# Kernel tuning notes

Hardware: AMD Instinct MI355X
Metric: run time of the kernel (lower is better)

The kernel has to match this reference:

```python
import jax, jax.numpy as jnp
import numpy as np
import itertools

KS = 5           # kernel_size per pseudo dim
PDIM = 2         # pseudo-coordinate dim
N_NODES = 50000
N_EDGES = 800000
D_IN = 128
D_OUT = 128
EPS = 1e-12


def l2norm(x):
    n = jnp.linalg.norm(x, axis=-1, keepdims=True)
    return x / jnp.maximum(n, EPS)


def spline_conv(x, src, dst, pseudo, weight, bias):
    """torch_spline_conv with degree=1, open splines, aggr='mean', no root weight."""
    N = x.shape[0]
    out_dim = weight.shape[-1]
    dim = pseudo.shape[1]
    v = pseudo * (KS - 1)                                   # [E, dim] in [0, KS-1)
    i0 = jnp.clip(jnp.floor(v), 0, KS - 2).astype(jnp.int32)
    frac = v - i0.astype(v.dtype)                           # [E, dim]
    # Precompute per-kernel transforms once per node: cheaper than per-edge GEMV
    Xk = jnp.einsum('ni,kio->nko', x, weight)               # [N, K=25, out]
    E = src.shape[0]
    y = jnp.zeros((E, out_dim), x.dtype)
    for bits in itertools.product((0, 1), repeat=dim):      # S = 2**dim = 4 combos
        b = jnp.ones((E,), x.dtype)
        wi = jnp.zeros((E,), jnp.int32)
        stride = 1
        for d, bit in enumerate(bits):
            b = b * (frac[:, d] if bit else 1.0 - frac[:, d])
            wi = wi + (i0[:, d] + bit) * stride
            stride *= KS
        y = y + b[:, None] * Xk[src, wi]                    # gather-weight per edge
    agg = jax.ops.segment_sum(y, dst, num_segments=N)       # scatter-add to targets
    deg = jax.ops.segment_sum(jnp.ones((E,), x.dtype), dst, num_segments=N)
    return agg / jnp.maximum(deg, 1.0)[:, None] + bias      # mean aggregation


def setup_inputs() -> dict:
    key = jax.random.key(0)
    ks = jax.random.split(key, 6)
    K = KS ** PDIM
    x = jax.random.normal(ks[0], (N_NODES, D_IN), jnp.float32)
    edge_index = jax.random.randint(ks[1], (2, N_EDGES), 0, N_NODES, jnp.int32)
    edge_attr = jax.random.uniform(ks[2], (N_EDGES, PDIM), jnp.float32)
    s0 = 1.0 / np.sqrt(K * D_IN)
    s1 = 1.0 / np.sqrt(K * D_OUT)
    w0 = jax.random.normal(ks[3], (K, D_IN, D_OUT), jnp.float32) * s0
    w1 = jax.random.normal(ks[4], (K, D_OUT, D_OUT), jnp.float32) * s1
    b0 = jnp.zeros((D_OUT,), jnp.float32)
    b1 = jnp.zeros((D_OUT,), jnp.float32)
    return {"x": x, "edge_index": edge_index, "edge_attr": edge_attr,
            "w0": w0, "b0": b0, "w1": w1, "b1": b1}


def reference(x, edge_index, edge_attr, w0, b0, w1, b1):
    src, dst = edge_index[0], edge_index[1]
    xs = [l2norm(x)]
    h = x
    for w, b in ((w0, b0), (w1, b1)):
        h = spline_conv(h, src, dst, edge_attr, w, b)
        xs.append(l2norm(h))
        h = jax.nn.relu(h)
    return jnp.concatenate(xs, axis=-1)                     # [N, D_IN + 2*D_OUT]
```

## Files before the change

### kernel.cpp

```cpp
#include <hip/hip_runtime.h>

#define D     128
#define OD    384
#define NK    25
#define KCMAX 13
#define KB0   13

typedef __attribute__((ext_vector_type(8))) short bf16x8;
typedef __attribute__((ext_vector_type(4))) float f32x4;
typedef __attribute__((ext_vector_type(4))) unsigned int u32x4;
typedef const __attribute__((address_space(1))) void gv_t;
typedef __attribute__((address_space(3))) void lv_t;

struct __align__(16) Rec {
  int src;
  unsigned int wi;
  unsigned int b01;
  unsigned int b23;
};

__device__ inline unsigned short f2bf(float f) {
  unsigned int u = __float_as_uint(f);
  u += 0x7fffu + ((u >> 16) & 1u);
  return (unsigned short)(u >> 16);
}
__device__ inline unsigned short f2h(float f) {
  return __builtin_bit_cast(unsigned short, (_Float16)f);
}
__device__ inline float h2f(unsigned int bits16) {
  return (float)__builtin_bit_cast(_Float16, (unsigned short)(bits16 & 0xffffu));
}


__device__ inline int edge_cls(int w00) {
  return (w00 + 6 < KB0) ? 0 : ((w00 >= KB0) ? 2 : 1);
}

__global__ __launch_bounds__(256) void count3_kernel(const int* __restrict__ dstA,
    const float* __restrict__ attr, int E, int* __restrict__ deg,
    int* __restrict__ cnt3) {
  int e = blockIdx.x * 256 + threadIdx.x;
  if (e >= E) return;
  int d = dstA[e];
  atomicAdd(&deg[d], 1);
  float v0 = attr[2 * e] * 4.0f;
  float v1 = attr[2 * e + 1] * 4.0f;
  int i0 = min(3, max(0, (int)v0));
  int i1 = min(3, max(0, (int)v1));
  int w00 = i0 + 5 * i1;
  atomicAdd(&cnt3[d * 3 + edge_cls(w00)], 1);
}


__global__ __launch_bounds__(1024) void scan_a_kernel(const int* __restrict__ cnt, int M,
    int* __restrict__ base3, int* __restrict__ bsum) {
  __shared__ int tmp[1024];
  int tid = threadIdx.x;
  int e = blockIdx.x * 1024 + tid;
  int v = (e < M) ? cnt[e] : 0;
  tmp[tid] = v;
  __syncthreads();
#pragma unroll
  for (int off = 1; off < 1024; off <<= 1) {
    int t = (tid >= off) ? tmp[tid - off] : 0;
    __syncthreads();
    tmp[tid] += t;
    __syncthreads();
  }
  if (e <= M) base3[e] = tmp[tid] - v;
  if (tid == 1023) bsum[blockIdx.x] = tmp[1023];
}

__global__ __launch_bounds__(256) void scan_b_kernel(int* __restrict__ bsum, int nblk) {
  __shared__ int tmp[256];
  __shared__ int carry;
  int tid = threadIdx.x;
  if (tid == 0) carry = 0;
  __syncthreads();
  for (int s = 0; s < nblk; s += 256) {
    int i = s + tid;
    int v = (i < nblk) ? bsum[i] : 0;
    tmp[tid] = v;
    __syncthreads();
#pragma unroll
    for (int off = 1; off < 256; off <<= 1) {
      int t = (tid >= off) ? tmp[tid - off] : 0;
      __syncthreads();
      tmp[tid] += t;
      __syncthreads();
    }
    if (i < nblk) bsum[i] = carry + tmp[tid] - v;
    __syncthreads();
    if (tid == 255) carry += tmp[255];
    __syncthreads();
  }
}

__global__ __launch_bounds__(256) void scan_c_kernel(int* __restrict__ base3,
    int* __restrict__ cursor, const int* __restrict__ bsum, int M) {
  int e = blockIdx.x * 256 + threadIdx.x;
  if (e > M) return;
  int v = base3[e] + bsum[e >> 10];
  base3[e] = v;
  if (e < M) cursor[e] = v;
}

__global__ __launch_bounds__(256) void fill_kernel(const int* __restrict__ srcA,
    const int* __restrict__ dstA, const float* __restrict__ attr, int E,
    int* __restrict__ cursor, Rec* __restrict__ recs) {
  int e = blockIdx.x * 256 + threadIdx.x;
  if (e >= E) return;
  int d = dstA[e];
  float v0 = attr[2 * e] * 4.0f;
  float v1 = attr[2 * e + 1] * 4.0f;
  int i0 = min(3, max(0, (int)v0));
  int i1 = min(3, max(0, (int)v1));
  float f0 = v0 - (float)i0;
  float f1 = v1 - (float)i1;
  int w00 = i0 + 5 * i1;
  int pos = atomicAdd(&cursor[d * 3 + edge_cls(w00)], 1);
  Rec r;
  r.src = srcA[e];
  unsigned int w = (unsigned int)w00;
  r.wi = w | ((w + 1) << 5) | ((w + 5) << 10) | ((w + 6) << 15);
  r.b01 = (unsigned int)f2h((1.f - f0) * (1.f - f1)) | ((unsigned int)f2h(f0 * (1.f - f1)) << 16);
  r.b23 = (unsigned int)f2h((1.f - f0) * f1) | ((unsigned int)f2h(f0 * f1) << 16);
  recs[pos] = r;
}

__global__ __launch_bounds__(256) void wt_kernel(const float* __restrict__ W0,
    const float* __restrict__ W1, unsigned short* __restrict__ WT0,
    unsigned short* __restrict__ WT1) {
  int idx = blockIdx.x * 256 + threadIdx.x;
  if (idx >= 128 * NK * D) return;
  const float* W = blockIdx.y ? W1 : W0;
  unsigned short* WT = blockIdx.y ? WT1 : WT0;
  int n = idx / (NK * D);
  int kk = idx - n * (NK * D);
  WT[idx] = f2bf(W[(size_t)kk * D + n]);
}


__global__ __launch_bounds__(256) void gather_kernel(const int* __restrict__ base3,
    const Rec* __restrict__ recs, const unsigned short* __restrict__ Xb,
    unsigned short* __restrict__ Gc, int N, int KCc, int kc0, int c_lo, int c_hi) {
  __shared__ float lacc[4][KCMAX * D];
  int w = threadIdx.x >> 6, l = threadIdx.x & 63;
  int dst = blockIdx.x * 4 + w;
  if (dst >= N) return;
  float* A = lacc[w];
  for (int k = 0; k < KCc; ++k)
    *(float2*)(A + k * D + l * 2) = make_float2(0.f, 0.f);

  const int l2 = l * 2;
  auto ACC = [&](const Rec& r, unsigned int xp) {
    float x0 = __uint_as_float(xp << 16);
    float x1 = __uint_as_float(xp & 0xffff0000u);
    float bq[4] = {h2f(r.b01), h2f(r.b01 >> 16), h2f(r.b23), h2f(r.b23 >> 16)};
#pragma unroll
    for (int q = 0; q < 4; ++q) {
      int k = (int)((r.wi >> (5 * q)) & 31u) - kc0;
      if ((unsigned)k < (unsigned)KCc) {
        float2 p = *(const float2*)(A + k * D + l2);
        p.x = fmaf(bq[q], x0, p.x);
        p.y = fmaf(bq[q], x1, p.y);
        *(float2*)(A + k * D + l2) = p;
      }
    }
  };

  int s = __builtin_amdgcn_readfirstlane(base3[dst * 3 + c_lo]);
  int e = __builtin_amdgcn_readfirstlane(base3[dst * 3 + c_hi]);
  if (s < e) {
    auto LD4 = [&](int j, Rec* rb) {
#pragma unroll
      for (int u = 0; u < 4; ++u) {
        int idx = (j + u < e) ? (j + u) : (e - 1);
        rb[u] = recs[idx];
        if (j + u >= e) { rb[u].b01 = 0u; rb[u].b23 = 0u; }
      }
    };
    Rec cur0, cur1, cur2, cur3;
    { Rec rb[4]; LD4(s, rb); cur0 = rb[0]; cur1 = rb[1]; cur2 = rb[2]; cur3 = rb[3]; }
    for (int j = s; j < e; j += 4) {
      unsigned int xp0 = *(const unsigned int*)(Xb + (size_t)cur0.src * D + l2);
      unsigned int xp1 = *(const unsigned int*)(Xb + (size_t)cur1.src * D + l2);
      unsigned int xp2 = *(const unsigned int*)(Xb + (size_t)cur2.src * D + l2);
      unsigned int xp3 = *(const unsigned int*)(Xb + (size_t)cur3.src * D + l2);
      bool more = (j + 4) < e;
      Rec nb[4];
      if (more) LD4(j + 4, nb);
      ACC(cur0, xp0); ACC(cur1, xp1); ACC(cur2, xp2); ACC(cur3, xp3);
      if (more) { cur0 = nb[0]; cur1 = nb[1]; cur2 = nb[2]; cur3 = nb[3]; }
    }
  }

  unsigned short* gr = Gc + (size_t)dst * ((size_t)KCc * D);
  for (int t = l; t < KCc * 16; t += 64) {
    const float* src = A + (t >> 4) * D + (t & 15) * 8;
    float4 v0 = *(const float4*)(src);
    float4 v1 = *(const float4*)(src + 4);
    u32x4 pk;
    pk[0] = (unsigned int)f2bf(v0.x) | ((unsigned int)f2bf(v0.y) << 16);
    pk[1] = (unsigned int)f2bf(v0.z) | ((unsigned int)f2bf(v0.w) << 16);
    pk[2] = (unsigned int)f2bf(v1.x) | ((unsigned int)f2bf(v1.y) << 16);
    pk[3] = (unsigned int)f2bf(v1.z) | ((unsigned int)f2bf(v1.w) << 16);
    *(u32x4*)(gr + (size_t)t * 8) = pk;
  }
}


__global__ __launch_bounds__(256) void gemm_kernel(
    const unsigned short* __restrict__ G, const unsigned short* __restrict__ WT,
    float* __restrict__ Y, int N, int KCc, int kc0, int first) {
  __shared__ __attribute__((aligned(16))) char At[2][16384];
  __shared__ __attribute__((aligned(16))) char Bt[2][16384];
  const int tid = threadIdx.x;
  const int w = tid >> 6;
  const int l = tid & 63;
  const int m0 = blockIdx.x * 128;
  const size_t ldG = (size_t)KCc * 256;
  const size_t ldW = (size_t)NK * 256;

  const int lrow = l >> 3;
  const int scol = ((l & 7) * 16) ^ (lrow << 4);

  f32x4 acc[2][8];
#pragma unroll
  for (int mr = 0; mr < 2; ++mr)
#pragma unroll
    for (int nc = 0; nc < 8; ++nc) {
      if (first) {
        acc[mr][nc] = (f32x4){0.f, 0.f, 0.f, 0.f};
      } else {
        int col = nc * 16 + (l & 15);
#pragma unroll
        for (int j = 0; j < 4; ++j) {
          int row = m0 + w * 32 + mr * 16 + (l >> 4) * 4 + j;
          acc[mr][nc][j] = (row < N) ? Y[(size_t)row * D + col] : 0.f;
        }
      }
    }

  const int steps = KCc * 2;
  auto STAGE = [&](int kt, int b) {
#pragma unroll
    for (int i = 0; i < 4; ++i) {
      int row = w * 32 + i * 8 + lrow;
      int node = m0 + row;
      if (node > N - 1) node = N - 1;
      const char* src = (const char*)G + (size_t)node * ldG + kt * 128 + scol;
      __builtin_amdgcn_global_load_lds((gv_t*)src, (lv_t*)(At[b] + (w * 4 + i) * 1024),
                                       16, 0, 0);
    }
#pragma unroll
    for (int i = 0; i < 4; ++i) {
      int nr = w * 32 + i * 8 + lrow;
      const char* src = (const char*)WT + (size_t)nr * ldW + kc0 * 256 + kt * 128 + scol;
      __builtin_amdgcn_global_load_lds((gv_t*)src, (lv_t*)(Bt[b] + (w * 4 + i) * 1024),
                                       16, 0, 0);
    }
  };

  STAGE(0, 0);
  __syncthreads();
  for (int kt = 0; kt < steps; ++kt) {
    const int cur = kt & 1;
    if (kt + 1 < steps) STAGE(kt + 1, cur ^ 1);
#pragma unroll
    for (int ks = 0; ks < 2; ++ks) {
      int kb = ks * 64 + (l >> 4) * 16;
      bf16x8 a[2], b[8];
#pragma unroll
      for (int mr = 0; mr < 2; ++mr) {
        int r = w * 32 + mr * 16 + (l & 15);
        a[mr] = *(const bf16x8*)(At[cur] + r * 128 + (kb ^ ((r & 7) << 4)));
      }
#pragma unroll
      for (int nc = 0; nc < 8; ++nc) {
        int nr = nc * 16 + (l & 15);
        b[nc] = *(const bf16x8*)(Bt[cur] + nr * 128 + (kb ^ ((nr & 7) << 4)));
      }
#pragma unroll
      for (int mr = 0; mr < 2; ++mr)
#pragma unroll
        for (int nc = 0; nc < 8; ++nc)
          acc[mr][nc] =
              __builtin_amdgcn_mfma_f32_16x16x32_bf16(a[mr], b[nc], acc[mr][nc], 0, 0, 0);
    }
    __syncthreads();
  }

#pragma unroll
  for (int mr = 0; mr < 2; ++mr)
#pragma unroll
    for (int nc = 0; nc < 8; ++nc) {
      int col = nc * 16 + (l & 15);
#pragma unroll
      for (int j = 0; j < 4; ++j) {
        int row = m0 + w * 32 + mr * 16 + (l >> 4) * 4 + j;
        if (row < N) Y[(size_t)row * D + col] = acc[mr][nc][j];
      }
    }
}


__global__ __launch_bounds__(256) void l2norm_x_kernel(const float* __restrict__ x,
    float* __restrict__ out, unsigned short* __restrict__ xbf, int N) {
  int g = blockIdx.x * 256 + threadIdx.x;
  int n = g >> 6, lane = g & 63;
  if (n >= N) return;
  float2 v = *(const float2*)(x + (size_t)n * D + lane * 2);
  float ss = v.x * v.x + v.y * v.y;
#pragma unroll
  for (int m = 1; m < 64; m <<= 1) ss += __shfl_xor(ss, m, 64);
  float r = 1.0f / fmaxf(sqrtf(ss), 1e-12f);
  *(float2*)(out + (size_t)n * OD + lane * 2) = make_float2(v.x * r, v.y * r);
  unsigned int pk = (unsigned int)f2bf(v.x) | ((unsigned int)f2bf(v.y) << 16);
  *(unsigned int*)(xbf + (size_t)n * D + lane * 2) = pk;
}

__global__ __launch_bounds__(256) void finalize_kernel(const float* __restrict__ y,
    const int* __restrict__ deg, const float* __restrict__ bias, float* __restrict__ out,
    unsigned short* __restrict__ xnext, int N) {
  int g = blockIdx.x * 256 + threadIdx.x;
  int n = g >> 6, lane = g & 63;
  if (n >= N) return;
  float inv = 1.0f / (float)max(deg[n], 1);
  float2 a = *(const float2*)(y + (size_t)n * D + lane * 2);
  float2 b = *(const float2*)(bias + lane * 2);
  float h0 = a.x * inv + b.x;
  float h1 = a.y * inv + b.y;
  float ss = h0 * h0 + h1 * h1;
#pragma unroll
  for (int m = 1; m < 64; m <<= 1) ss += __shfl_xor(ss, m, 64);
  float r = 1.0f / fmaxf(sqrtf(ss), 1e-12f);
  *(float2*)(out + (size_t)n * OD + lane * 2) = make_float2(h0 * r, h1 * r);
  if (xnext) {
    unsigned int pk = (unsigned int)f2bf(fmaxf(h0, 0.f)) |
                      ((unsigned int)f2bf(fmaxf(h1, 0.f)) << 16);
    *(unsigned int*)(xnext + (size_t)n * D + lane * 2) = pk;
  }
}


extern "C" void kernel_launch(void* const* d_in, const int* in_sizes, int n_in,
                              void* d_out, int out_size, void* d_ws, size_t ws_size,
                              hipStream_t stream) {
  const float* x    = (const float*)d_in[0];
  const int*   ei   = (const int*)d_in[1];
  const float* attr = (const float*)d_in[2];
  const float* w0   = (const float*)d_in[3];
  const float* b0   = (const float*)d_in[4];
  const float* w1   = (const float*)d_in[5];
  const float* b1   = (const float*)d_in[6];
  float* out = (float*)d_out;

  const int N = in_sizes[0] / D;
  const int E = in_sizes[1] / 2;
  const int* srcA = ei;
  const int* dstA = ei + E;
  const int M3 = N * 3;

  char* p = (char*)d_ws;
  auto carve = [&](size_t bytes) -> char* {
    char* r = p;
    p += (bytes + 255) & ~(size_t)255;
    return r;
  };
  unsigned short* xbf    = (unsigned short*)carve((size_t)N * D * 2);
  unsigned short* xtmp   = (unsigned short*)carve((size_t)N * D * 2);
  float*          ygemm  = (float*)carve((size_t)N * D * 4);
  int*            deg    = (int*)carve((size_t)N * 4);
  int*            cnt3   = (int*)carve((size_t)M3 * 4);
  int*            base3  = (int*)carve(((size_t)M3 + 1) * 4);
  int*            cursor = (int*)carve((size_t)M3 * 4);
  int*            bsum   = (int*)carve(4096);
  Rec*            recs   = (Rec*)carve((size_t)E * sizeof(Rec));
  unsigned short* WT0    = (unsigned short*)carve((size_t)128 * NK * D * 2);
  unsigned short* WT1    = (unsigned short*)carve((size_t)128 * NK * D * 2);
  size_t used = (size_t)(p - (char*)d_ws);
  size_t remain = (ws_size > used) ? (ws_size - used) : 0;
  int KCg = (int)(remain / ((size_t)N * D * 2));
  if (KCg > KCMAX) KCg = KCMAX;
  if (KCg < 1) KCg = 1;
  unsigned short* Gc = (unsigned short*)carve((size_t)N * (size_t)KCg * D * 2);
  (void)n_in; (void)out_size;

  hipMemsetAsync(deg, 0, (size_t)N * 4, stream);
  hipMemsetAsync(cnt3, 0, (size_t)M3 * 4, stream);

  int eb = (E + 255) / 256;
  count3_kernel<<<eb, 256, 0, stream>>>(dstA, attr, E, deg, cnt3);
  int nblk_a = (M3 + 1 + 1023) / 1024;
  scan_a_kernel<<<nblk_a, 1024, 0, stream>>>(cnt3, M3, base3, bsum);
  scan_b_kernel<<<1, 256, 0, stream>>>(bsum, nblk_a);
  scan_c_kernel<<<(M3 + 1 + 255) / 256, 256, 0, stream>>>(base3, cursor, bsum, M3);
  fill_kernel<<<eb, 256, 0, stream>>>(srcA, dstA, attr, E, cursor, recs);
  int wtb = (128 * NK * D + 255) / 256;
  wt_kernel<<<dim3(wtb, 2), 256, 0, stream>>>(w0, w1, WT0, WT1);

  int nb = (N * 64 + 255) / 256;
  l2norm_x_kernel<<<nb, 256, 0, stream>>>(x, out, xbf, N);

  int gbg = (N + 3) / 4;
  int gbm = (N + 127) / 128;
  const unsigned short* xin = xbf;
  const float* Bv[2] = {b0, b1};
  const unsigned short* WTl[2] = {WT0, WT1};
  for (int layer = 0; layer < 2; ++layer) {
    if (KCg >= KB0) {
      gather_kernel<<<gbg, 256, 0, stream>>>(base3, recs, xin, Gc, N, KB0, 0, 0, 2);
      gemm_kernel<<<gbm, 256, 0, stream>>>(Gc, WTl[layer], ygemm, N, KB0, 0, 1);
      gather_kernel<<<gbg, 256, 0, stream>>>(base3, recs, xin, Gc, N, NK - KB0, KB0, 1, 3);
      gemm_kernel<<<gbm, 256, 0, stream>>>(Gc, WTl[layer], ygemm, N, NK - KB0, KB0, 0);
    } else {
      int first = 1;
      for (int kc0 = 0; kc0 < NK; kc0 += KCg) {
        int KCc = min(KCg, NK - kc0);
        gather_kernel<<<gbg, 256, 0, stream>>>(base3, recs, xin, Gc, N, KCc, kc0, 0, 3);
        gemm_kernel<<<gbm, 256, 0, stream>>>(Gc, WTl[layer], ygemm, N, KCc, kc0, first);
        first = 0;
      }
    }
    finalize_kernel<<<nb, 256, 0, stream>>>(ygemm, deg, Bv[layer], out + D * (layer + 1),
                                            layer == 0 ? xtmp : nullptr, N);
    xin = xtmp;
  }
}
```

Measured before the change: 627.6 us.

## Bucket edges per (dst, kernel index) and accumulate gather in registers

Replaces the 3-class per-destination edge bucketing with a full CSR over (dst, kernel-weight index), storing four (src, basis weight) records per edge. The gather kernel walks each of the 25 buckets in turn and accumulates into registers instead of doing read-modify-write on shared-memory accumulators per edge. In exchange it needs four times as many records, 25x larger counters and scan arrays, four atomics per edge, and it gathers each source row up to four times. The old fixed 13/12 split is dropped in favour of a generic chunk loop.

```diff
diff --git a/kernel.cpp b/kernel.cpp
--- a/kernel.cpp
+++ b/kernel.cpp
@@ -4,41 +4,22 @@
 #define OD    384
 #define NK    25
 #define KCMAX 13
-#define KB0   13
 
 typedef __attribute__((ext_vector_type(8))) short bf16x8;
 typedef __attribute__((ext_vector_type(4))) float f32x4;
-typedef __attribute__((ext_vector_type(4))) unsigned int u32x4;
 typedef const __attribute__((address_space(1))) void gv_t;
 typedef __attribute__((address_space(3))) void lv_t;
-
-struct __align__(16) Rec {
-  int src;
-  unsigned int wi;
-  unsigned int b01;
-  unsigned int b23;
-};
 
 __device__ inline unsigned short f2bf(float f) {
   unsigned int u = __float_as_uint(f);
   u += 0x7fffu + ((u >> 16) & 1u);
   return (unsigned short)(u >> 16);
 }
-__device__ inline unsigned short f2h(float f) {
-  return __builtin_bit_cast(unsigned short, (_Float16)f);
-}
-__device__ inline float h2f(unsigned int bits16) {
-  return (float)__builtin_bit_cast(_Float16, (unsigned short)(bits16 & 0xffffu));
-}
-
-
-__device__ inline int edge_cls(int w00) {
-  return (w00 + 6 < KB0) ? 0 : ((w00 >= KB0) ? 2 : 1);
-}
-
-__global__ __launch_bounds__(256) void count3_kernel(const int* __restrict__ dstA,
+
+
+__global__ __launch_bounds__(256) void count25_kernel(const int* __restrict__ dstA,
     const float* __restrict__ attr, int E, int* __restrict__ deg,
-    int* __restrict__ cnt3) {
+    int* __restrict__ cnt25) {
   int e = blockIdx.x * 256 + threadIdx.x;
   if (e >= E) return;
   int d = dstA[e];
@@ -47,13 +28,16 @@
   float v1 = attr[2 * e + 1] * 4.0f;
   int i0 = min(3, max(0, (int)v0));
   int i1 = min(3, max(0, (int)v1));
-  int w00 = i0 + 5 * i1;
-  atomicAdd(&cnt3[d * 3 + edge_cls(w00)], 1);
+  int b = d * NK + i0 + 5 * i1;
+  atomicAdd(&cnt25[b], 1);
+  atomicAdd(&cnt25[b + 1], 1);
+  atomicAdd(&cnt25[b + 5], 1);
+  atomicAdd(&cnt25[b + 6], 1);
 }
 
 
 __global__ __launch_bounds__(1024) void scan_a_kernel(const int* __restrict__ cnt, int M,
-    int* __restrict__ base3, int* __restrict__ bsum) {
+    int* __restrict__ base, int* __restrict__ bsum) {
   __shared__ int tmp[1024];
   int tid = threadIdx.x;
   int e = blockIdx.x * 1024 + tid;
@@ -67,7 +51,7 @@
     tmp[tid] += t;
     __syncthreads();
   }
-  if (e <= M) base3[e] = tmp[tid] - v;
+  if (e <= M) base[e] = tmp[tid] - v;
   if (tid == 1023) bsum[blockIdx.x] = tmp[1023];
 }
 
@@ -96,36 +80,38 @@
   }
 }
 
-__global__ __launch_bounds__(256) void scan_c_kernel(int* __restrict__ base3,
+__global__ __launch_bounds__(256) void scan_c_kernel(int* __restrict__ base,
     int* __restrict__ cursor, const int* __restrict__ bsum, int M) {
   int e = blockIdx.x * 256 + threadIdx.x;
   if (e > M) return;
-  int v = base3[e] + bsum[e >> 10];
-  base3[e] = v;
+  int v = base[e] + bsum[e >> 10];
+  base[e] = v;
   if (e < M) cursor[e] = v;
 }
 
-__global__ __launch_bounds__(256) void fill_kernel(const int* __restrict__ srcA,
+__global__ __launch_bounds__(256) void fill25_kernel(const int* __restrict__ srcA,
     const int* __restrict__ dstA, const float* __restrict__ attr, int E,
-    int* __restrict__ cursor, Rec* __restrict__ recs) {
+    int* __restrict__ cursor, uint2* __restrict__ recs) {
   int e = blockIdx.x * 256 + threadIdx.x;
   if (e >= E) return;
-  int d = dstA[e];
+  int s = srcA[e], d = dstA[e];
   float v0 = attr[2 * e] * 4.0f;
   float v1 = attr[2 * e + 1] * 4.0f;
   int i0 = min(3, max(0, (int)v0));
   int i1 = min(3, max(0, (int)v1));
   float f0 = v0 - (float)i0;
   float f1 = v1 - (float)i1;
-  int w00 = i0 + 5 * i1;
-  int pos = atomicAdd(&cursor[d * 3 + edge_cls(w00)], 1);
-  Rec r;
-  r.src = srcA[e];
-  unsigned int w = (unsigned int)w00;
-  r.wi = w | ((w + 1) << 5) | ((w + 5) << 10) | ((w + 6) << 15);
-  r.b01 = (unsigned int)f2h((1.f - f0) * (1.f - f1)) | ((unsigned int)f2h(f0 * (1.f - f1)) << 16);
-  r.b23 = (unsigned int)f2h((1.f - f0) * f1) | ((unsigned int)f2h(f0 * f1) << 16);
-  recs[pos] = r;
+  int b = d * NK + i0 + 5 * i1;
+  unsigned int su = (unsigned int)s;
+  int p;
+  p = atomicAdd(&cursor[b], 1);
+  recs[p] = make_uint2(su, __float_as_uint((1.f - f0) * (1.f - f1)));
+  p = atomicAdd(&cursor[b + 1], 1);
+  recs[p] = make_uint2(su, __float_as_uint(f0 * (1.f - f1)));
+  p = atomicAdd(&cursor[b + 5], 1);
+  recs[p] = make_uint2(su, __float_as_uint((1.f - f0) * f1));
+  p = atomicAdd(&cursor[b + 6], 1);
+  recs[p] = make_uint2(su, __float_as_uint(f0 * f1));
 }
 
 __global__ __launch_bounds__(256) void wt_kernel(const float* __restrict__ W0,
@@ -141,71 +127,52 @@
 }
 
 
-__global__ __launch_bounds__(256) void gather_kernel(const int* __restrict__ base3,
-    const Rec* __restrict__ recs, const unsigned short* __restrict__ Xb,
-    unsigned short* __restrict__ Gc, int N, int KCc, int kc0, int c_lo, int c_hi) {
-  __shared__ float lacc[4][KCMAX * D];
+__global__ __launch_bounds__(256) void gather_kernel(const int* __restrict__ base25,
+    const uint2* __restrict__ recs, const unsigned short* __restrict__ Xb,
+    unsigned short* __restrict__ Gc, int N, int KCc, int kc0) {
   int w = threadIdx.x >> 6, l = threadIdx.x & 63;
   int dst = blockIdx.x * 4 + w;
   if (dst >= N) return;
-  float* A = lacc[w];
-  for (int k = 0; k < KCc; ++k)
-    *(float2*)(A + k * D + l * 2) = make_float2(0.f, 0.f);
-
   const int l2 = l * 2;
-  auto ACC = [&](const Rec& r, unsigned int xp) {
-    float x0 = __uint_as_float(xp << 16);
-    float x1 = __uint_as_float(xp & 0xffff0000u);
-    float bq[4] = {h2f(r.b01), h2f(r.b01 >> 16), h2f(r.b23), h2f(r.b23 >> 16)};
-#pragma unroll
-    for (int q = 0; q < 4; ++q) {
-      int k = (int)((r.wi >> (5 * q)) & 31u) - kc0;
-      if ((unsigned)k < (unsigned)KCc) {
-        float2 p = *(const float2*)(A + k * D + l2);
-        p.x = fmaf(bq[q], x0, p.x);
-        p.y = fmaf(bq[q], x1, p.y);
-        *(float2*)(A + k * D + l2) = p;
-      }
-    }
-  };
-
-  int s = __builtin_amdgcn_readfirstlane(base3[dst * 3 + c_lo]);
-  int e = __builtin_amdgcn_readfirstlane(base3[dst * 3 + c_hi]);
-  if (s < e) {
-    auto LD4 = [&](int j, Rec* rb) {
-#pragma unroll
-      for (int u = 0; u < 4; ++u) {
-        int idx = (j + u < e) ? (j + u) : (e - 1);
-        rb[u] = recs[idx];
-        if (j + u >= e) { rb[u].b01 = 0u; rb[u].b23 = 0u; }
-      }
-    };
-    Rec cur0, cur1, cur2, cur3;
-    { Rec rb[4]; LD4(s, rb); cur0 = rb[0]; cur1 = rb[1]; cur2 = rb[2]; cur3 = rb[3]; }
-    for (int j = s; j < e; j += 4) {
-      unsigned int xp0 = *(const unsigned int*)(Xb + (size_t)cur0.src * D + l2);
-      unsigned int xp1 = *(const unsigned int*)(Xb + (size_t)cur1.src * D + l2);
-      unsigned int xp2 = *(const unsigned int*)(Xb + (size_t)cur2.src * D + l2);
-      unsigned int xp3 = *(const unsigned int*)(Xb + (size_t)cur3.src * D + l2);
-      bool more = (j + 4) < e;
-      Rec nb[4];
-      if (more) LD4(j + 4, nb);
-      ACC(cur0, xp0); ACC(cur1, xp1); ACC(cur2, xp2); ACC(cur3, xp3);
-      if (more) { cur0 = nb[0]; cur1 = nb[1]; cur2 = nb[2]; cur3 = nb[3]; }
-    }
+  const int* bp = base25 + dst * NK + kc0;
+
+  float2 accv[KCMAX];
+#pragma unroll
+  for (int kk = 0; kk < KCMAX; ++kk) {
+    float2 a = make_float2(0.f, 0.f);
+    if (kk < KCc) {
+      int g0 = __builtin_amdgcn_readfirstlane(bp[kk]);
+      int g1 = __builtin_amdgcn_readfirstlane(bp[kk + 1]);
+      for (int j = g0; j < g1; j += 4) {
+        uint2 r[4];
+        unsigned int xp[4];
+#pragma unroll
+        for (int u = 0; u < 4; ++u) {
+          int idx = (j + u < g1) ? (j + u) : (g1 - 1);
+          r[u] = recs[idx];
+        }
+#pragma unroll
+        for (int u = 0; u < 4; ++u)
+          xp[u] = *(const unsigned int*)(Xb + (size_t)r[u].x * D + l2);
+#pragma unroll
+        for (int u = 0; u < 4; ++u) {
+          float b = (j + u < g1) ? __uint_as_float(r[u].y) : 0.f;
+          a.x = fmaf(b, __uint_as_float(xp[u] << 16), a.x);
+          a.y = fmaf(b, __uint_as_float(xp[u] & 0xffff0000u), a.y);
+        }
+      }
+    }
+    accv[kk] = a;
   }
 
   unsigned short* gr = Gc + (size_t)dst * ((size_t)KCc * D);
-  for (int t = l; t < KCc * 16; t += 64) {
-    const float* src = A + (t >> 4) * D + (t & 15) * 8;
-    float4 v0 = *(const float4*)(src);
-    float4 v1 = *(const float4*)(src + 4);
-    u32x4 pk;
-    pk[0] = (unsigned int)f2bf(v0.x) | ((unsigned int)f2bf(v0.y) << 16);
-    pk[1] = (unsigned int)f2bf(v0.z) | ((unsigned int)f2bf(v0.w) << 16);
-    pk[2] = (unsigned int)f2bf(v1.x) | ((unsigned int)f2bf(v1.y) << 16);
-    pk[3] = (unsigned int)f2bf(v1.z) | ((unsigned int)f2bf(v1.w) << 16);
-    *(u32x4*)(gr + (size_t)t * 8) = pk;
+#pragma unroll
+  for (int kk = 0; kk < KCMAX; ++kk) {
+    if (kk < KCc) {
+      unsigned int pk =
+          (unsigned int)f2bf(accv[kk].x) | ((unsigned int)f2bf(accv[kk].y) << 16);
+      *(unsigned int*)(gr + kk * D + l2) = pk;
+    }
   }
 }
 
@@ -360,7 +327,7 @@
   const int E = in_sizes[1] / 2;
   const int* srcA = ei;
   const int* dstA = ei + E;
-  const int M3 = N * 3;
+  const int M25 = N * NK;
 
   char* p = (char*)d_ws;
   auto carve = [&](size_t bytes) -> char* {
@@ -372,11 +339,11 @@
   unsigned short* xtmp   = (unsigned short*)carve((size_t)N * D * 2);
   float*          ygemm  = (float*)carve((size_t)N * D * 4);
   int*            deg    = (int*)carve((size_t)N * 4);
-  int*            cnt3   = (int*)carve((size_t)M3 * 4);
-  int*            base3  = (int*)carve(((size_t)M3 + 1) * 4);
-  int*            cursor = (int*)carve((size_t)M3 * 4);
-  int*            bsum   = (int*)carve(4096);
-  Rec*            recs   = (Rec*)carve((size_t)E * sizeof(Rec));
+  int*            cnt25  = (int*)carve((size_t)M25 * 4);
+  int*            base25 = (int*)carve(((size_t)M25 + 1) * 4);
+  int*            cursor = (int*)carve((size_t)M25 * 4);
+  int*            bsum   = (int*)carve(8192);
+  uint2*          recs   = (uint2*)carve((size_t)E * 4 * 8);
   unsigned short* WT0    = (unsigned short*)carve((size_t)128 * NK * D * 2);
   unsigned short* WT1    = (unsigned short*)carve((size_t)128 * NK * D * 2);
   size_t used = (size_t)(p - (char*)d_ws);
@@ -388,15 +355,15 @@
   (void)n_in; (void)out_size;
 
   hipMemsetAsync(deg, 0, (size_t)N * 4, stream);
-  hipMemsetAsync(cnt3, 0, (size_t)M3 * 4, stream);
+  hipMemsetAsync(cnt25, 0, (size_t)M25 * 4, stream);
 
   int eb = (E + 255) / 256;
-  count3_kernel<<<eb, 256, 0, stream>>>(dstA, attr, E, deg, cnt3);
-  int nblk_a = (M3 + 1 + 1023) / 1024;
-  scan_a_kernel<<<nblk_a, 1024, 0, stream>>>(cnt3, M3, base3, bsum);
+  count25_kernel<<<eb, 256, 0, stream>>>(dstA, attr, E, deg, cnt25);
+  int nblk_a = (M25 + 1 + 1023) / 1024;
+  scan_a_kernel<<<nblk_a, 1024, 0, stream>>>(cnt25, M25, base25, bsum);
   scan_b_kernel<<<1, 256, 0, stream>>>(bsum, nblk_a);
-  scan_c_kernel<<<(M3 + 1 + 255) / 256, 256, 0, stream>>>(base3, cursor, bsum, M3);
-  fill_kernel<<<eb, 256, 0, stream>>>(srcA, dstA, attr, E, cursor, recs);
+  scan_c_kernel<<<(M25 + 1 + 255) / 256, 256, 0, stream>>>(base25, cursor, bsum, M25);
+  fill25_kernel<<<eb, 256, 0, stream>>>(srcA, dstA, attr, E, cursor, recs);
   int wtb = (128 * NK * D + 255) / 256;
   wt_kernel<<<dim3(wtb, 2), 256, 0, stream>>>(w0, w1, WT0, WT1);
 
@@ -409,19 +376,12 @@
   const float* Bv[2] = {b0, b1};
   const unsigned short* WTl[2] = {WT0, WT1};
   for (int layer = 0; layer < 2; ++layer) {
-    if (KCg >= KB0) {
-      gather_kernel<<<gbg, 256, 0, stream>>>(base3, recs, xin, Gc, N, KB0, 0, 0, 2);
-      gemm_kernel<<<gbm, 256, 0, stream>>>(Gc, WTl[layer], ygemm, N, KB0, 0, 1);
-      gather_kernel<<<gbg, 256, 0, stream>>>(base3, recs, xin, Gc, N, NK - KB0, KB0, 1, 3);
-      gemm_kernel<<<gbm, 256, 0, stream>>>(Gc, WTl[layer], ygemm, N, NK - KB0, KB0, 0);
-    } else {
-      int first = 1;
-      for (int kc0 = 0; kc0 < NK; kc0 += KCg) {
-        int KCc = min(KCg, NK - kc0);
-        gather_kernel<<<gbg, 256, 0, stream>>>(base3, recs, xin, Gc, N, KCc, kc0, 0, 3);
-        gemm_kernel<<<gbm, 256, 0, stream>>>(Gc, WTl[layer], ygemm, N, KCc, kc0, first);
-        first = 0;
-      }
+    int first = 1;
+    for (int kc0 = 0; kc0 < NK; kc0 += KCg) {
+      int KCc = min(KCg, NK - kc0);
+      gather_kernel<<<gbg, 256, 0, stream>>>(base25, recs, xin, Gc, N, KCc, kc0);
+      gemm_kernel<<<gbm, 256, 0, stream>>>(Gc, WTl[layer], ygemm, N, KCc, kc0, first);
+      first = 0;
     }
     finalize_kernel<<<nb, 256, 0, stream>>>(ygemm, deg, Bv[layer], out + D * (layer + 1),
                                             layer == 0 ? xtmp : nullptr, N);
```

Result: slower. 1.081 ms (+72.2%).

## Schedule gather waves over destination nodes sorted by descending degree

Applied to the files above, without the earlier changes.

Adds a counting sort of destination nodes by in-degree (histogram, single-block scan, scatter) to build a permutation, and has the gather kernel assign each wave to perm[wid] instead of its linear index. Blocks then process nodes of similar degree together, with heavy nodes first, to reduce intra-block imbalance and tail effects. It costs three extra small kernels and a memset, and loses the locality of writing consecutive destination rows to Gc.

```diff
diff --git a/kernel.cpp b/kernel.cpp
--- a/kernel.cpp
+++ b/kernel.cpp
@@ -5,6 +5,7 @@
 #define NK    25
 #define KCMAX 13
 #define KB0   13
+#define DB    1024
 
 typedef __attribute__((ext_vector_type(8))) short bf16x8;
 typedef __attribute__((ext_vector_type(4))) float f32x4;
@@ -128,6 +129,40 @@
   recs[pos] = r;
 }
 
+
+__global__ __launch_bounds__(256) void dhist_kernel(const int* __restrict__ deg, int N,
+                                                    int* __restrict__ hist) {
+  int d = blockIdx.x * 256 + threadIdx.x;
+  if (d >= N) return;
+  int key = (DB - 1) - min(deg[d], DB - 1);
+  atomicAdd(&hist[key], 1);
+}
+
+__global__ __launch_bounds__(1024) void dscan_kernel(const int* __restrict__ hist,
+                                                     int* __restrict__ dcur) {
+  __shared__ int tmp[DB];
+  int tid = threadIdx.x;
+  int v = hist[tid];
+  tmp[tid] = v;
+  __syncthreads();
+#pragma unroll
+  for (int off = 1; off < DB; off <<= 1) {
+    int t = (tid >= off) ? tmp[tid - off] : 0;
+    __syncthreads();
+    tmp[tid] += t;
+    __syncthreads();
+  }
+  dcur[tid] = tmp[tid] - v;
+}
+
+__global__ __launch_bounds__(256) void dscatter_kernel(const int* __restrict__ deg, int N,
+    int* __restrict__ dcur, int* __restrict__ perm) {
+  int d = blockIdx.x * 256 + threadIdx.x;
+  if (d >= N) return;
+  int key = (DB - 1) - min(deg[d], DB - 1);
+  perm[atomicAdd(&dcur[key], 1)] = d;
+}
+
 __global__ __launch_bounds__(256) void wt_kernel(const float* __restrict__ W0,
     const float* __restrict__ W1, unsigned short* __restrict__ WT0,
     unsigned short* __restrict__ WT1) {
@@ -143,11 +178,13 @@
 
 __global__ __launch_bounds__(256) void gather_kernel(const int* __restrict__ base3,
     const Rec* __restrict__ recs, const unsigned short* __restrict__ Xb,
-    unsigned short* __restrict__ Gc, int N, int KCc, int kc0, int c_lo, int c_hi) {
+    unsigned short* __restrict__ Gc, int N, int KCc, int kc0, int c_lo, int c_hi,
+    const int* __restrict__ perm) {
   __shared__ float lacc[4][KCMAX * D];
   int w = threadIdx.x >> 6, l = threadIdx.x & 63;
-  int dst = blockIdx.x * 4 + w;
-  if (dst >= N) return;
+  int wid = blockIdx.x * 4 + w;
+  if (wid >= N) return;
+  int dst = __builtin_amdgcn_readfirstlane(perm[wid]);
   float* A = lacc[w];
   for (int k = 0; k < KCc; ++k)
     *(float2*)(A + k * D + l * 2) = make_float2(0.f, 0.f);
@@ -376,6 +413,9 @@
   int*            base3  = (int*)carve(((size_t)M3 + 1) * 4);
   int*            cursor = (int*)carve((size_t)M3 * 4);
   int*            bsum   = (int*)carve(4096);
+  int*            hist   = (int*)carve(DB * 4);
+  int*            dcur   = (int*)carve(DB * 4);
+  int*            perm   = (int*)carve((size_t)N * 4);
   Rec*            recs   = (Rec*)carve((size_t)E * sizeof(Rec));
   unsigned short* WT0    = (unsigned short*)carve((size_t)128 * NK * D * 2);
   unsigned short* WT1    = (unsigned short*)carve((size_t)128 * NK * D * 2);
@@ -389,14 +429,19 @@
 
   hipMemsetAsync(deg, 0, (size_t)N * 4, stream);
   hipMemsetAsync(cnt3, 0, (size_t)M3 * 4, stream);
+  hipMemsetAsync(hist, 0, DB * 4, stream);
 
   int eb = (E + 255) / 256;
+  int nb256 = (N + 255) / 256;
   count3_kernel<<<eb, 256, 0, stream>>>(dstA, attr, E, deg, cnt3);
   int nblk_a = (M3 + 1 + 1023) / 1024;
   scan_a_kernel<<<nblk_a, 1024, 0, stream>>>(cnt3, M3, base3, bsum);
   scan_b_kernel<<<1, 256, 0, stream>>>(bsum, nblk_a);
   scan_c_kernel<<<(M3 + 1 + 255) / 256, 256, 0, stream>>>(base3, cursor, bsum, M3);
   fill_kernel<<<eb, 256, 0, stream>>>(srcA, dstA, attr, E, cursor, recs);
+  dhist_kernel<<<nb256, 256, 0, stream>>>(deg, N, hist);
+  dscan_kernel<<<1, DB, 0, stream>>>(hist, dcur);
+  dscatter_kernel<<<nb256, 256, 0, stream>>>(deg, N, dcur, perm);
   int wtb = (128 * NK * D + 255) / 256;
   wt_kernel<<<dim3(wtb, 2), 256, 0, stream>>>(w0, w1, WT0, WT1);
 
@@ -410,15 +455,17 @@
   const unsigned short* WTl[2] = {WT0, WT1};
   for (int layer = 0; layer < 2; ++layer) {
     if (KCg >= KB0) {
-      gather_kernel<<<gbg, 256, 0, stream>>>(base3, recs, xin, Gc, N, KB0, 0, 0, 2);
+      gather_kernel<<<gbg, 256, 0, stream>>>(base3, recs, xin, Gc, N, KB0, 0, 0, 2, perm);
       gemm_kernel<<<gbm, 256, 0, stream>>>(Gc, WTl[layer], ygemm, N, KB0, 0, 1);
-      gather_kernel<<<gbg, 256, 0, stream>>>(base3, recs, xin, Gc, N, NK - KB0, KB0, 1, 3);
+      gather_kernel<<<gbg, 256, 0, stream>>>(base3, recs, xin, Gc, N, NK - KB0, KB0, 1, 3,
+                                             perm);
       gemm_kernel<<<gbm, 256, 0, stream>>>(Gc, WTl[layer], ygemm, N, NK - KB0, KB0, 0);
     } else {
       int first = 1;
       for (int kc0 = 0; kc0 < NK; kc0 += KCg) {
         int KCc = min(KCg, NK - kc0);
-        gather_kernel<<<gbg, 256, 0, stream>>>(base3, recs, xin, Gc, N, KCc, kc0, 0, 3);
+        gather_kernel<<<gbg, 256, 0, stream>>>(base3, recs, xin, Gc, N, KCc, kc0, 0, 3,
+                                               perm);
         gemm_kernel<<<gbm, 256, 0, stream>>>(Gc, WTl[layer], ygemm, N, KCc, kc0, first);
         first = 0;
       }
```

Result: slower. 899.8 us (+43.4%).
